# Kernel tuning notes

Hardware: AMD Instinct MI355X
Metric: run time of the kernel (lower is better)

The kernel has to match this reference:

```python
import jax, jax.numpy as jnp
import numpy as np

HIDDEN = 1024
HEADS = 16
HEAD_DIM = HIDDEN // HEADS

def setup_inputs() -> dict:
    key = jax.random.key(0)
    k1, k2, k3 = jax.random.split(key, 3)
    scale = 1.0 / np.sqrt(HIDDEN)
    return {
        "x": jax.random.normal(k1, (2, 2048, HIDDEN), dtype=jnp.float32),
        "w_qkv": jax.random.normal(k2, (HIDDEN, 3 * HIDDEN), dtype=jnp.float32) * scale,
        "b_qkv": jnp.zeros((3 * HIDDEN,), dtype=jnp.float32),
        "w_out": jax.random.normal(k3, (HIDDEN, HIDDEN), dtype=jnp.float32) * scale,
        "b_out": jnp.zeros((HIDDEN,), dtype=jnp.float32),
    }

def reference(x, w_qkv, b_qkv, w_out, b_out):
    B, S, H = x.shape
    qkv = x @ w_qkv + b_qkv                              # (B,S,3H)
    qkv = qkv.reshape(B, S, 3, HEADS, HEAD_DIM)
    qkv = jnp.transpose(qkv, (2, 0, 3, 1, 4))            # (3,B,nh,S,hd)
    q, k, v = qkv[0], qkv[1], qkv[2]
    scores = jnp.einsum("bhqd,bhkd->bhqk", q, k) / np.sqrt(HEAD_DIM)
    causal = jnp.triu(jnp.ones((S, S), dtype=bool), k=1)  # True above diagonal
    scores = jnp.where(causal, -jnp.inf, scores)
    attn = jax.nn.softmax(scores, axis=-1)               # dropout: eval mode (identity)
    out = jnp.einsum("bhqk,bhkd->bhqd", attn, v)
    out = jnp.transpose(out, (0, 2, 1, 3)).reshape(B, S, H)
    return out @ w_out + b_out
```

## Files before the change

kernel.cpp:

```cpp
#include <hip/hip_runtime.h>
#include <hip/hip_bf16.h>

typedef short short8 __attribute__((ext_vector_type(8)));
typedef float f32x4 __attribute__((ext_vector_type(4)));

typedef const __attribute__((address_space(1))) unsigned int* gas_ptr;
typedef __attribute__((address_space(3))) unsigned int* las_ptr;
#define ASYNC16(g, l) __builtin_amdgcn_global_load_lds((gas_ptr)(g), (las_ptr)(l), 16, 0, 0)

__device__ __forceinline__ unsigned short f2bf(float f) {
    unsigned int u = __builtin_bit_cast(unsigned int, f);
    u += 0x7fff + ((u >> 16) & 1);
    return (unsigned short)(u >> 16);
}
__device__ __forceinline__ float bf2f(unsigned short s) {
    unsigned int u = (unsigned int)s << 16;
    return __builtin_bit_cast(float, u);
}
__device__ __forceinline__ unsigned int pkbf_trunc(float lo, float hi) {
    return __builtin_amdgcn_perm(__builtin_bit_cast(unsigned int, hi),
                                 __builtin_bit_cast(unsigned int, lo), 0x07060302u);
}

__device__ __forceinline__ void transpose_tile(
    const float* __restrict__ w, unsigned short* __restrict__ wt,
    int K, int N, int k0, int n0, unsigned short* tile)
{
    for (int i = threadIdx.x; i < 64 * 64; i += 256) {
        int r = i >> 6, c = i & 63;
        tile[r * 65 + c] = f2bf(w[(size_t)(k0 + r) * N + n0 + c]);
    }
    __syncthreads();
    for (int i = threadIdx.x; i < 64 * 64; i += 256) {
        int r = i >> 6, c = i & 63;
        wt[(size_t)(n0 + r) * K + k0 + c] = tile[c * 65 + r];
    }
}

__global__ __launch_bounds__(256) void prep(
    const float* __restrict__ x, const float* __restrict__ w_qkv,
    const float* __restrict__ w_out,
    unsigned short* __restrict__ x_b, unsigned short* __restrict__ wqkv_t,
    unsigned short* __restrict__ wout_t)
{
    __shared__ unsigned short tile[64 * 65];
    int bid = blockIdx.x;
    if (bid < 4096) {
        int i = (bid * 256 + threadIdx.x) * 4;
        float4 v = *(const float4*)(x + i);
        ushort4 o;
        o.x = f2bf(v.x); o.y = f2bf(v.y); o.z = f2bf(v.z); o.w = f2bf(v.w);
        *(ushort4*)(x_b + i) = o;
    } else if (bid < 4096 + 768) {
        int t = bid - 4096;
        transpose_tile(w_qkv, wqkv_t, 1024, 3072, (t / 48) * 64, (t % 48) * 64, tile);
    } else {
        int t = bid - 4864;
        transpose_tile(w_out, wout_t, 1024, 1024, (t >> 4) * 64, (t & 15) * 64, tile);
    }
}


template<bool OUT_BF16, bool QKV>
__global__ __launch_bounds__(256, 3) void gemm_bt(
    const unsigned short* __restrict__ A,
    const unsigned short* __restrict__ Bt,
    const float* __restrict__ bias,
    void* __restrict__ C,
    unsigned short* __restrict__ vTp,
    int M, int N, int K)
{
    __shared__ __align__(16) unsigned short As[128 * 32];
    __shared__ __align__(16) unsigned short Bs[128 * 32];
    const int tid = threadIdx.x;
    const int lane = tid & 63;
    const int wave = tid >> 6;
    const int wr = wave >> 1, wc = wave & 1;
    const int m0 = blockIdx.x * 128, n0 = blockIdx.y * 128;
    const int fr = lane & 15, fq = lane >> 4;

    f32x4 acc[4][4] = {};

    const int grow = lane >> 2;
    const int gcol = (lane & 3) * 8;
    const unsigned short* Ag = A  + (size_t)(m0 + wave * 32 + grow) * K + gcol;
    const unsigned short* Bg = Bt + (size_t)(n0 + wave * 32 + grow) * K + gcol;
    unsigned short* AsW0 = As + (wave * 32) * 32;
    unsigned short* AsW1 = As + (wave * 32 + 16) * 32;
    unsigned short* BsW0 = Bs + (wave * 32) * 32;
    unsigned short* BsW1 = Bs + (wave * 32 + 16) * 32;

    for (int k0 = 0; k0 < K; k0 += 32) {
        __syncthreads();
        ASYNC16(Ag + k0,          AsW0);
        ASYNC16(Ag + 16 * K + k0, AsW1);
        ASYNC16(Bg + k0,          BsW0);
        ASYNC16(Bg + 16 * K + k0, BsW1);
        __syncthreads();

        short8 af[4], bfr[4];
#pragma unroll
        for (int i = 0; i < 4; i++)
            af[i] = *(const short8*)(As + (wr * 64 + i * 16 + fr) * 32 + fq * 8);
#pragma unroll
        for (int j = 0; j < 4; j++)
            bfr[j] = *(const short8*)(Bs + (wc * 64 + j * 16 + fr) * 32 + fq * 8);
#pragma unroll
        for (int i = 0; i < 4; i++)
#pragma unroll
            for (int j = 0; j < 4; j++)
                acc[i][j] = __builtin_amdgcn_mfma_f32_16x16x32_bf16(af[i], bfr[j], acc[i][j], 0, 0, 0);
    }

#pragma unroll
    for (int i = 0; i < 4; i++)
#pragma unroll
        for (int j = 0; j < 4; j++) {
            int col = n0 + wc * 64 + j * 16 + fr;
            float bv = bias[col];
            if (QKV && col >= 2048) {
                int hh = (col - 2048) >> 6, d = col & 63;
#pragma unroll
                for (int r = 0; r < 4; r++) {
                    int row = m0 + wr * 64 + i * 16 + fq * 4 + r;
                    int bb = row >> 11, s = row & 2047;
                    vTp[((size_t)(bb * 16 + hh) * 64 + d) * 2048 + s] = f2bf(acc[i][j][r] + bv);
                }
            } else {
                const int cstride = QKV ? 2048 : N;
#pragma unroll
                for (int r = 0; r < 4; r++) {
                    int row = m0 + wr * 64 + i * 16 + fq * 4 + r;
                    float v = acc[i][j][r] + bv;
                    if (OUT_BF16)
                        ((unsigned short*)C)[(size_t)row * cstride + col] = f2bf(v);
                    else
                        ((float*)C)[(size_t)row * cstride + col] = v;
                }
            }
        }
}


template<int RG0>
__device__ __forceinline__ void attn_step(
    const unsigned short* __restrict__ Ks0, const unsigned short* __restrict__ Ks1,
    const unsigned short* __restrict__ Vs0, const unsigned short* __restrict__ Vs1,
    unsigned short* __restrict__ Psw,
    const short8 (&qf)[4][2], const short8 ones,
    f32x4 (&o_acc)[4][4], f32x4 (&l_acc)[4],
    int j0, int fr, int fq,
    const int (&qrow0)[4], bool diagA, bool diagB)
{
    short8 kf[4][2];
#pragma unroll
    for (int t = 0; t < 4; t++) {
        kf[t][0] = *(const short8*)(Ks0 + (t * 16 + fr) * 32 + fq * 8);
        kf[t][1] = *(const short8*)(Ks1 + (t * 16 + fr) * 32 + fq * 8);
    }

#pragma unroll
    for (int rg = RG0; rg < 4; rg++) {
        f32x4 s[4];
#pragma unroll
        for (int t = 0; t < 4; t++) {
            s[t] = (f32x4){0.f, 0.f, 0.f, 0.f};
            s[t] = __builtin_amdgcn_mfma_f32_16x16x32_bf16(qf[rg][0], kf[t][0], s[t], 0, 0, 0);
            s[t] = __builtin_amdgcn_mfma_f32_16x16x32_bf16(qf[rg][1], kf[t][1], s[t], 0, 0, 0);
        }
        const bool diag = (rg < 2) ? diagA : diagB;
        unsigned short* prow = Psw + rg * (16 * 64);
        if (diag) {
#pragma unroll
            for (int t = 0; t < 4; t++) {
                float p[4];
#pragma unroll
                for (int r = 0; r < 4; r++) {
                    float v = __expf(s[t][r] * 0.125f - 8.0f);
                    if ((j0 + t * 16 + fr) > (qrow0[rg] + fq * 4 + r)) v = 0.f;
                    p[r] = v;
                }
                unsigned int pk01 = pkbf_trunc(p[0], p[1]);
                unsigned int pk23 = pkbf_trunc(p[2], p[3]);
                int base = (fq * 4) * 64 + ((t * 16 + fr + 16 * fq) & 63);
                prow[base]       = (unsigned short)pk01;
                prow[base + 64]  = (unsigned short)(pk01 >> 16);
                prow[base + 128] = (unsigned short)pk23;
                prow[base + 192] = (unsigned short)(pk23 >> 16);
            }
        } else {
#pragma unroll
            for (int t = 0; t < 4; t++) {
                float p[4];
#pragma unroll
                for (int r = 0; r < 4; r++)
                    p[r] = __expf(s[t][r] * 0.125f - 8.0f);
                unsigned int pk01 = pkbf_trunc(p[0], p[1]);
                unsigned int pk23 = pkbf_trunc(p[2], p[3]);
                int base = (fq * 4) * 64 + ((t * 16 + fr + 16 * fq) & 63);
                prow[base]       = (unsigned short)pk01;
                prow[base + 64]  = (unsigned short)(pk01 >> 16);
                prow[base + 128] = (unsigned short)pk23;
                prow[base + 192] = (unsigned short)(pk23 >> 16);
            }
        }
    }

#pragma unroll
    for (int ks = 0; ks < 2; ks++) {
        const unsigned short* Vsb = ks ? Vs1 : Vs0;
        const int colp = (ks * 32 + fq * 8 + 16 * ((fr >> 2) & 3)) & 63;
        short8 pf[4];
#pragma unroll
        for (int rg = RG0; rg < 4; rg++)
            pf[rg] = *(const short8*)(Psw + rg * (16 * 64) + fr * 64 + colp);
#pragma unroll
        for (int t = 0; t < 4; t++) {
            short8 vf = *(const short8*)(Vsb + (t * 16 + fr) * 32 + fq * 8);
#pragma unroll
            for (int rg = RG0; rg < 4; rg++)
                o_acc[rg][t] = __builtin_amdgcn_mfma_f32_16x16x32_bf16(pf[rg], vf, o_acc[rg][t], 0, 0, 0);
        }
#pragma unroll
        for (int rg = RG0; rg < 4; rg++)
            l_acc[rg] = __builtin_amdgcn_mfma_f32_16x16x32_bf16(pf[rg], ones, l_acc[rg], 0, 0, 0);
    }
}

__global__ __launch_bounds__(128, 2) void flash_attn(
    const unsigned short* __restrict__ qkv,
    const unsigned short* __restrict__ vT,
    unsigned short* __restrict__ Opart,
    float* __restrict__ lpart)
{
    const int p = blockIdx.x;
    const int g = blockIdx.y;
    const int h = blockIdx.z & 15, b = blockIdx.z >> 4;
    const int tid = threadIdx.x, wave = tid >> 6, lane = tid & 63;
    const int fr = lane & 15, fq = lane >> 4;
    const size_t RS = 2048;

    const unsigned short* Qb = qkv + (size_t)b * 2048 * RS + h * 64;
    const unsigned short* Kb = Qb + 1024;
    const unsigned short* Vt = vT + (size_t)(b * 16 + h) * 64 * 2048;

    __shared__ __align__(16) unsigned short Ks[2][64 * 32];
    __shared__ __align__(16) unsigned short Vs[2][64 * 32];
    __shared__ __align__(16) unsigned short Ps[2][4 * 16 * 64];

    short8 qf[4][2];
    int qrow0[4];
#pragma unroll
    for (int rg = 0; rg < 4; rg++) {
        int qt = (rg < 2) ? p : (31 - p);
        qrow0[rg] = qt * 64 + wave * 32 + (rg & 1) * 16;
        const unsigned short* qrow = Qb + (size_t)(qrow0[rg] + fr) * RS;
        qf[rg][0] = *(const short8*)(qrow + fq * 8);
        qf[rg][1] = *(const short8*)(qrow + 32 + fq * 8);
    }
    short8 ones;
#pragma unroll
    for (int e = 0; e < 8; e++) ones[e] = (short)0x3F80;

    f32x4 o_acc[4][4] = {};
    f32x4 l_acc[4] = {};

    const int grow = lane >> 2;
    const int gcol = (lane & 3) * 8;
    const unsigned short* Kg = Kb + (size_t)(wave * 32 + grow) * RS + gcol;
    const unsigned short* Vg = Vt + (size_t)(wave * 32 + grow) * 2048 + gcol;
    unsigned short* KsW00 = Ks[0] + (wave * 32) * 32;
    unsigned short* KsW01 = Ks[0] + (wave * 32 + 16) * 32;
    unsigned short* KsW10 = Ks[1] + (wave * 32) * 32;
    unsigned short* KsW11 = Ks[1] + (wave * 32 + 16) * 32;
    unsigned short* VsW00 = Vs[0] + (wave * 32) * 32;
    unsigned short* VsW01 = Vs[0] + (wave * 32 + 16) * 32;
    unsigned short* VsW10 = Vs[1] + (wave * 32) * 32;
    unsigned short* VsW11 = Vs[1] + (wave * 32 + 16) * 32;

    const int mid = (p >= 8) ? 8 : (16 - p);
    const int lo = g ? mid : 0;
    const int hi = g ? (32 - p) : mid;

    for (int jt = lo; jt < hi; jt++) {
        const int j0 = jt * 64;
        __syncthreads();
        ASYNC16(Kg + (size_t)j0 * RS,               KsW00);
        ASYNC16(Kg + (size_t)(j0 + 16) * RS,        KsW01);
        ASYNC16(Kg + (size_t)j0 * RS + 32,          KsW10);
        ASYNC16(Kg + (size_t)(j0 + 16) * RS + 32,   KsW11);
        ASYNC16(Vg + j0,               VsW00);
        ASYNC16(Vg + 16 * 2048 + j0,   VsW01);
        ASYNC16(Vg + j0 + 32,          VsW10);
        ASYNC16(Vg + 16 * 2048 + j0 + 32, VsW11);
        __syncthreads();

        bool diagA = (jt == p), diagB = (jt == 31 - p);
        if (jt <= p)
            attn_step<0>(Ks[0], Ks[1], Vs[0], Vs[1], Ps[wave], qf, ones,
                         o_acc, l_acc, j0, fr, fq, qrow0, diagA, diagB);
        else
            attn_step<2>(Ks[0], Ks[1], Vs[0], Vs[1], Ps[wave], qf, ones,
                         o_acc, l_acc, j0, fr, fq, qrow0, diagA, diagB);
    }

    unsigned short* Og = Opart + (size_t)g * 4096 * 1024;
    float* lg = lpart + (size_t)g * 4096 * 16;
#pragma unroll
    for (int rg = 0; rg < 4; rg++) {
#pragma unroll
        for (int t = 0; t < 4; t++)
#pragma unroll
            for (int r = 0; r < 4; r++) {
                int row = qrow0[rg] + fq * 4 + r;
                Og[(size_t)(b * 2048 + row) * 1024 + h * 64 + t * 16 + fr] = f2bf(o_acc[rg][t][r]);
            }
        if (fr == 0) {
#pragma unroll
            for (int r = 0; r < 4; r++) {
                int row = qrow0[rg] + fq * 4 + r;
                lg[(size_t)(b * 2048 + row) * 16 + h] = l_acc[rg][r];
            }
        }
    }
}

__global__ __launch_bounds__(256) void reduce_attn(
    const unsigned short* __restrict__ Opart, const float* __restrict__ lpart,
    unsigned short* __restrict__ out)
{
    int i = (blockIdx.x * 256 + threadIdx.x) * 8;
    int row = i >> 10, h = (i & 1023) >> 6;
    float lsum = lpart[(size_t)row * 16 + h] + lpart[(size_t)4096 * 16 + row * 16 + h];
    float inv = 1.0f / lsum;
    ushort4 a0 = *(const ushort4*)(Opart + i);
    ushort4 a1 = *(const ushort4*)(Opart + i + 4);
    ushort4 b0 = *(const ushort4*)(Opart + (size_t)4096 * 1024 + i);
    ushort4 b1 = *(const ushort4*)(Opart + (size_t)4096 * 1024 + i + 4);
    ushort4 o0, o1;
    o0.x = f2bf((bf2f(a0.x) + bf2f(b0.x)) * inv);
    o0.y = f2bf((bf2f(a0.y) + bf2f(b0.y)) * inv);
    o0.z = f2bf((bf2f(a0.z) + bf2f(b0.z)) * inv);
    o0.w = f2bf((bf2f(a0.w) + bf2f(b0.w)) * inv);
    o1.x = f2bf((bf2f(a1.x) + bf2f(b1.x)) * inv);
    o1.y = f2bf((bf2f(a1.y) + bf2f(b1.y)) * inv);
    o1.z = f2bf((bf2f(a1.z) + bf2f(b1.z)) * inv);
    o1.w = f2bf((bf2f(a1.w) + bf2f(b1.w)) * inv);
    *(ushort4*)(out + i) = o0;
    *(ushort4*)(out + i + 4) = o1;
}

extern "C" void kernel_launch(void* const* d_in, const int* in_sizes, int n_in,
                              void* d_out, int out_size, void* d_ws, size_t ws_size,
                              hipStream_t stream) {
    const float* x      = (const float*)d_in[0];
    const float* w_qkv  = (const float*)d_in[1];
    const float* b_qkv  = (const float*)d_in[2];
    const float* w_out  = (const float*)d_in[3];
    const float* b_out  = (const float*)d_in[4];
    float* out = (float*)d_out;

    char* ws = (char*)d_ws;
    unsigned short* x_b    = (unsigned short*)(ws);
    unsigned short* wqkv_t = (unsigned short*)(ws + 8u  * 1024 * 1024);
    unsigned short* wout_t = (unsigned short*)(ws + 14u * 1024 * 1024);
    unsigned short* qkv    = (unsigned short*)(ws + 16u * 1024 * 1024);
    unsigned short* attn   = (unsigned short*)(ws + 32u * 1024 * 1024);
    unsigned short* vT     = (unsigned short*)(ws + 40u * 1024 * 1024);
    unsigned short* Opart  = (unsigned short*)(ws + 48u * 1024 * 1024);
    float*          lpart  = (float*)         (ws + 64u * 1024 * 1024);

    prep<<<5120, 256, 0, stream>>>(x, w_qkv, w_out, x_b, wqkv_t, wout_t);
    gemm_bt<true, true ><<<dim3(32, 24), 256, 0, stream>>>(x_b,  wqkv_t, b_qkv, qkv, vT, 4096, 3072, 1024);
    flash_attn<<<dim3(16, 2, 32), 128, 0, stream>>>(qkv, vT, Opart, lpart);
    reduce_attn<<<2048, 256, 0, stream>>>(Opart, lpart, attn);
    gemm_bt<false, false><<<dim3(32, 8),  256, 0, stream>>>(attn, wout_t, b_out, out, nullptr, 4096, 1024, 1024);
}
```

Before: 193.2 us.

## Split attention KV range four ways, swizzle LDS, use exp2 and MFMA priority

Each (p, head) attention block's KV range is now split four ways instead of two, with a cost-balanced split that weights diagonal-pair tiles differently. This doubles the flash_attn grid to fill more CUs, and reduce_attn now sums four partials. The K/V/P shared-memory layouts get XOR-style swizzles, the QK MFMA operands are swapped so P is stored as 8-byte vector writes, exp is computed with a native exp2 and folded constants, and s_setprio wraps the MFMA sections. The cost is more partial-output traffic, a larger workspace and a heavier reduce pass.

```diff
diff --git a/kernel.cpp b/kernel.cpp
--- a/kernel.cpp
+++ b/kernel.cpp
@@ -20,6 +20,13 @@
 __device__ __forceinline__ unsigned int pkbf_trunc(float lo, float hi) {
     return __builtin_amdgcn_perm(__builtin_bit_cast(unsigned int, hi),
                                  __builtin_bit_cast(unsigned int, lo), 0x07060302u);
+}
+__device__ __forceinline__ float fexp2(float x) {
+#if __has_builtin(__builtin_amdgcn_exp2f)
+    return __builtin_amdgcn_exp2f(x);
+#else
+    return __expf(x * 0.6931471805599453f);
+#endif
 }
 
 __device__ __forceinline__ void transpose_tile(
@@ -152,56 +159,60 @@
     int j0, int fr, int fq,
     const int (&qrow0)[4], bool diagA, bool diagB)
 {
+    const int kpos = ((fq + (fr >> 1)) & 3) * 8;
     short8 kf[4][2];
 #pragma unroll
     for (int t = 0; t < 4; t++) {
-        kf[t][0] = *(const short8*)(Ks0 + (t * 16 + fr) * 32 + fq * 8);
-        kf[t][1] = *(const short8*)(Ks1 + (t * 16 + fr) * 32 + fq * 8);
-    }
+        kf[t][0] = *(const short8*)(Ks0 + (t * 16 + fr) * 32 + kpos);
+        kf[t][1] = *(const short8*)(Ks1 + (t * 16 + fr) * 32 + kpos);
+    }
+
+    const float C1 = 0.18033688011112042f;
+    const float C2 = -11.541560327111707f;
 
 #pragma unroll
     for (int rg = RG0; rg < 4; rg++) {
         f32x4 s[4];
+        __builtin_amdgcn_s_setprio(1);
 #pragma unroll
         for (int t = 0; t < 4; t++) {
             s[t] = (f32x4){0.f, 0.f, 0.f, 0.f};
-            s[t] = __builtin_amdgcn_mfma_f32_16x16x32_bf16(qf[rg][0], kf[t][0], s[t], 0, 0, 0);
-            s[t] = __builtin_amdgcn_mfma_f32_16x16x32_bf16(qf[rg][1], kf[t][1], s[t], 0, 0, 0);
-        }
+            s[t] = __builtin_amdgcn_mfma_f32_16x16x32_bf16(kf[t][0], qf[rg][0], s[t], 0, 0, 0);
+            s[t] = __builtin_amdgcn_mfma_f32_16x16x32_bf16(kf[t][1], qf[rg][1], s[t], 0, 0, 0);
+        }
+        __builtin_amdgcn_s_setprio(0);
         const bool diag = (rg < 2) ? diagA : diagB;
         unsigned short* prow = Psw + rg * (16 * 64);
+        const int qr = qrow0[rg] + fr;
         if (diag) {
+#pragma unroll
+            for (int t = 0; t < 4; t++) {
+                const int kb = j0 + t * 16 + fq * 4;
+                float p[4];
+#pragma unroll
+                for (int r = 0; r < 4; r++) {
+                    float v = fexp2(s[t][r] * C1 + C2);
+                    if (kb + r > qr) v = 0.f;
+                    p[r] = v;
+                }
+                uint2 pk;
+                pk.x = pkbf_trunc(p[0], p[1]);
+                pk.y = pkbf_trunc(p[2], p[3]);
+                const int blk = (t * 2 + (fq >> 1) + fr) & 7;
+                *(uint2*)(prow + fr * 64 + blk * 8 + (fq & 1) * 4) = pk;
+            }
+        } else {
 #pragma unroll
             for (int t = 0; t < 4; t++) {
                 float p[4];
 #pragma unroll
-                for (int r = 0; r < 4; r++) {
-                    float v = __expf(s[t][r] * 0.125f - 8.0f);
-                    if ((j0 + t * 16 + fr) > (qrow0[rg] + fq * 4 + r)) v = 0.f;
-                    p[r] = v;
-                }
-                unsigned int pk01 = pkbf_trunc(p[0], p[1]);
-                unsigned int pk23 = pkbf_trunc(p[2], p[3]);
-                int base = (fq * 4) * 64 + ((t * 16 + fr + 16 * fq) & 63);
-                prow[base]       = (unsigned short)pk01;
-                prow[base + 64]  = (unsigned short)(pk01 >> 16);
-                prow[base + 128] = (unsigned short)pk23;
-                prow[base + 192] = (unsigned short)(pk23 >> 16);
-            }
-        } else {
-#pragma unroll
-            for (int t = 0; t < 4; t++) {
-                float p[4];
-#pragma unroll
                 for (int r = 0; r < 4; r++)
-                    p[r] = __expf(s[t][r] * 0.125f - 8.0f);
-                unsigned int pk01 = pkbf_trunc(p[0], p[1]);
-                unsigned int pk23 = pkbf_trunc(p[2], p[3]);
-                int base = (fq * 4) * 64 + ((t * 16 + fr + 16 * fq) & 63);
-                prow[base]       = (unsigned short)pk01;
-                prow[base + 64]  = (unsigned short)(pk01 >> 16);
-                prow[base + 128] = (unsigned short)pk23;
-                prow[base + 192] = (unsigned short)(pk23 >> 16);
+                    p[r] = fexp2(s[t][r] * C1 + C2);
+                uint2 pk;
+                pk.x = pkbf_trunc(p[0], p[1]);
+                pk.y = pkbf_trunc(p[2], p[3]);
+                const int blk = (t * 2 + (fq >> 1) + fr) & 7;
+                *(uint2*)(prow + fr * 64 + blk * 8 + (fq & 1) * 4) = pk;
             }
         }
     }
@@ -209,14 +220,15 @@
 #pragma unroll
     for (int ks = 0; ks < 2; ks++) {
         const unsigned short* Vsb = ks ? Vs1 : Vs0;
-        const int colp = (ks * 32 + fq * 8 + 16 * ((fr >> 2) & 3)) & 63;
+        const int colp = ((ks * 4 + fq + fr) & 7) * 8;
         short8 pf[4];
 #pragma unroll
         for (int rg = RG0; rg < 4; rg++)
             pf[rg] = *(const short8*)(Psw + rg * (16 * 64) + fr * 64 + colp);
+        __builtin_amdgcn_s_setprio(1);
 #pragma unroll
         for (int t = 0; t < 4; t++) {
-            short8 vf = *(const short8*)(Vsb + (t * 16 + fr) * 32 + fq * 8);
+            short8 vf = *(const short8*)(Vsb + (t * 16 + fr) * 32 + kpos);
 #pragma unroll
             for (int rg = RG0; rg < 4; rg++)
                 o_acc[rg][t] = __builtin_amdgcn_mfma_f32_16x16x32_bf16(pf[rg], vf, o_acc[rg][t], 0, 0, 0);
@@ -224,6 +236,7 @@
 #pragma unroll
         for (int rg = RG0; rg < 4; rg++)
             l_acc[rg] = __builtin_amdgcn_mfma_f32_16x16x32_bf16(pf[rg], ones, l_acc[rg], 0, 0, 0);
+        __builtin_amdgcn_s_setprio(0);
     }
 }
 
@@ -266,7 +279,7 @@
     f32x4 l_acc[4] = {};
 
     const int grow = lane >> 2;
-    const int gcol = (lane & 3) * 8;
+    const int gcol = (((lane & 3) - (grow >> 1)) & 3) * 8;
     const unsigned short* Kg = Kb + (size_t)(wave * 32 + grow) * RS + gcol;
     const unsigned short* Vg = Vt + (size_t)(wave * 32 + grow) * 2048 + gcol;
     unsigned short* KsW00 = Ks[0] + (wave * 32) * 32;
@@ -278,9 +291,10 @@
     unsigned short* VsW10 = Vs[1] + (wave * 32) * 32;
     unsigned short* VsW11 = Vs[1] + (wave * 32 + 16) * 32;
 
-    const int mid = (p >= 8) ? 8 : (16 - p);
-    const int lo = g ? mid : 0;
-    const int hi = g ? (32 - p) : mid;
+    const int c8 = 8 * (p + 1);
+    const int T0 = g * 33, T1 = T0 + 33;
+    const int lo = (T0 <= c8) ? ((T0 + 4) >> 3) : (p + 1 + ((T0 - c8 + 2) >> 2));
+    const int hi = (T1 <= c8) ? ((T1 + 4) >> 3) : (p + 1 + ((T1 - c8 + 2) >> 2));
 
     for (int jt = lo; jt < hi; jt++) {
         const int j0 = jt * 64;
@@ -289,9 +303,9 @@
         ASYNC16(Kg + (size_t)(j0 + 16) * RS,        KsW01);
         ASYNC16(Kg + (size_t)j0 * RS + 32,          KsW10);
         ASYNC16(Kg + (size_t)(j0 + 16) * RS + 32,   KsW11);
-        ASYNC16(Vg + j0,               VsW00);
-        ASYNC16(Vg + 16 * 2048 + j0,   VsW01);
-        ASYNC16(Vg + j0 + 32,          VsW10);
+        ASYNC16(Vg + j0,                  VsW00);
+        ASYNC16(Vg + 16 * 2048 + j0,      VsW01);
+        ASYNC16(Vg + j0 + 32,             VsW10);
         ASYNC16(Vg + 16 * 2048 + j0 + 32, VsW11);
         __syncthreads();
 
@@ -331,21 +345,25 @@
 {
     int i = (blockIdx.x * 256 + threadIdx.x) * 8;
     int row = i >> 10, h = (i & 1023) >> 6;
-    float lsum = lpart[(size_t)row * 16 + h] + lpart[(size_t)4096 * 16 + row * 16 + h];
+    float lsum = 0.f;
+#pragma unroll
+    for (int g = 0; g < 4; g++)
+        lsum += lpart[(size_t)g * 4096 * 16 + row * 16 + h];
     float inv = 1.0f / lsum;
-    ushort4 a0 = *(const ushort4*)(Opart + i);
-    ushort4 a1 = *(const ushort4*)(Opart + i + 4);
-    ushort4 b0 = *(const ushort4*)(Opart + (size_t)4096 * 1024 + i);
-    ushort4 b1 = *(const ushort4*)(Opart + (size_t)4096 * 1024 + i + 4);
+    float acc[8] = {0.f, 0.f, 0.f, 0.f, 0.f, 0.f, 0.f, 0.f};
+#pragma unroll
+    for (int g = 0; g < 4; g++) {
+        const unsigned short* Op = Opart + (size_t)g * 4096 * 1024 + i;
+        ushort4 a0 = *(const ushort4*)(Op);
+        ushort4 a1 = *(const ushort4*)(Op + 4);
+        acc[0] += bf2f(a0.x); acc[1] += bf2f(a0.y); acc[2] += bf2f(a0.z); acc[3] += bf2f(a0.w);
+        acc[4] += bf2f(a1.x); acc[5] += bf2f(a1.y); acc[6] += bf2f(a1.z); acc[7] += bf2f(a1.w);
+    }
     ushort4 o0, o1;
-    o0.x = f2bf((bf2f(a0.x) + bf2f(b0.x)) * inv);
-    o0.y = f2bf((bf2f(a0.y) + bf2f(b0.y)) * inv);
-    o0.z = f2bf((bf2f(a0.z) + bf2f(b0.z)) * inv);
-    o0.w = f2bf((bf2f(a0.w) + bf2f(b0.w)) * inv);
-    o1.x = f2bf((bf2f(a1.x) + bf2f(b1.x)) * inv);
-    o1.y = f2bf((bf2f(a1.y) + bf2f(b1.y)) * inv);
-    o1.z = f2bf((bf2f(a1.z) + bf2f(b1.z)) * inv);
-    o1.w = f2bf((bf2f(a1.w) + bf2f(b1.w)) * inv);
+    o0.x = f2bf(acc[0] * inv); o0.y = f2bf(acc[1] * inv);
+    o0.z = f2bf(acc[2] * inv); o0.w = f2bf(acc[3] * inv);
+    o1.x = f2bf(acc[4] * inv); o1.y = f2bf(acc[5] * inv);
+    o1.z = f2bf(acc[6] * inv); o1.w = f2bf(acc[7] * inv);
     *(ushort4*)(out + i) = o0;
     *(ushort4*)(out + i + 4) = o1;
 }
@@ -368,11 +386,11 @@
     unsigned short* attn   = (unsigned short*)(ws + 32u * 1024 * 1024);
     unsigned short* vT     = (unsigned short*)(ws + 40u * 1024 * 1024);
     unsigned short* Opart  = (unsigned short*)(ws + 48u * 1024 * 1024);
-    float*          lpart  = (float*)         (ws + 64u * 1024 * 1024);
+    float*          lpart  = (float*)         (ws + 80u * 1024 * 1024);
 
     prep<<<5120, 256, 0, stream>>>(x, w_qkv, w_out, x_b, wqkv_t, wout_t);
     gemm_bt<true, true ><<<dim3(32, 24), 256, 0, stream>>>(x_b,  wqkv_t, b_qkv, qkv, vT, 4096, 3072, 1024);
-    flash_attn<<<dim3(16, 2, 32), 128, 0, stream>>>(qkv, vT, Opart, lpart);
+    flash_attn<<<dim3(16, 4, 32), 128, 0, stream>>>(qkv, vT, Opart, lpart);
     reduce_attn<<<2048, 256, 0, stream>>>(Opart, lpart, attn);
     gemm_bt<false, false><<<dim3(32, 8),  256, 0, stream>>>(attn, wout_t, b_out, out, nullptr, 4096, 1024, 1024);
 }
```

Measured after the change: 196.9 us. No clear change (+1.9%).
